# Optimization experiments

Measured on AMD Instinct MI355X. Metric: run time of the kernel, lower is better.

The kernel has to match this reference:

```python
import jax, jax.numpy as jnp
import numpy as np

B, IDF, RES = 32, 64, 128
CDF, SRC_L, A_DIM = 768, 18, 100
QUERY_L = RES * RES


def setup_inputs() -> dict:
    key = jax.random.key(0)
    ks = jax.random.split(key, 5)
    inputs = jax.random.normal(ks[0], (B, IDF, RES, RES), dtype=jnp.float32)
    context = jax.random.normal(ks[1], (B, CDF, SRC_L), dtype=jnp.float32)
    conv_ctx_w = jax.random.normal(ks[2], (IDF, CDF), dtype=jnp.float32) * (1.0 / np.sqrt(CDF))
    conv_w = jax.random.normal(ks[3], (IDF,), dtype=jnp.float32) * (1.0 / np.sqrt(IDF))
    conv_b = jnp.zeros((1,), dtype=jnp.float32)
    fc_w = jax.random.normal(ks[4], (A_DIM, QUERY_L), dtype=jnp.float32) * (1.0 / np.sqrt(QUERY_L))
    fc_b = jnp.zeros((A_DIM,), dtype=jnp.float32)
    return {"inputs": inputs, "context": context, "conv_ctx_w": conv_ctx_w,
            "conv_w": conv_w, "conv_b": conv_b, "fc_w": fc_w, "fc_b": fc_b}


def reference(inputs, context, conv_ctx_w, conv_w, conv_b, fc_w, fc_b):
    b, idf, ih, iw = inputs.shape
    queryL = ih * iw
    # target: [b, idf, queryL]
    target = inputs.reshape(b, idf, queryL)
    # 1x1 conv on context (conv_context): [b, idf, sourceL]
    sourceT = jnp.einsum('ic,bcs->bis', conv_ctx_w, context)
    # attn scores: [b, queryL, sourceL]; softmax over sourceL (dim=1 on flattened view)
    attn = jnp.einsum('biq,bis->bqs', target, sourceT)
    attn = jax.nn.softmax(attn, axis=-1)
    # weighted context: [b, idf, queryL]
    wctx = jnp.einsum('bis,bqs->biq', sourceT, attn)
    # 1x1 conv to single channel (self.conv): [b, queryL]
    wctx = jnp.einsum('i,biq->bq', conv_w, wctx) + conv_b
    # att_fc: [b, a_dim]
    out = wctx @ fc_w.T + fc_b
    return out
```

## Files before the change

kernel.cpp:

```cpp
#include <hip/hip_runtime.h>

#define BB 32
#define IDF 64
#define QL 16384
#define CDF 768
#define SL 18
#define SLP 20
#define CLP 21
#define ADIM 100

typedef __attribute__((address_space(3))) unsigned int lds_u32_t;
typedef __attribute__((address_space(1))) const unsigned int glb_u32_t;

__global__ __launch_bounds__(256, 2) void kA_source(
        const float* __restrict__ ctx,
        const float* __restrict__ wic,
        const float* __restrict__ fc_b,
        float* __restrict__ sT,
        float* __restrict__ out)
{
    __shared__ float ctx_l[CDF * CLP];
    const int blk  = blockIdx.x;
    const int tid  = threadIdx.x;
    const int wave = tid >> 6;
    const int lane = tid & 63;
    const int b = blk >> 4;
    const int g = blk & 15;

    if (blk < 13) {
        const int t = blk * 256 + tid;
        if (t < BB * ADIM) out[t] = fc_b[t % ADIM];
    }

    const float* ctxb = ctx + (size_t)b * CDF * SL;
    for (int t = tid; t < CDF * SL; t += 256) {
        const int c = t / SL;
        const int s = t - c * SL;
        ctx_l[c * CLP + s] = ctxb[t];
    }
    __syncthreads();

    const int i = g * 4 + wave;
    const float* wrow = wic + (size_t)i * CDF;

    float acc[SL];
#pragma unroll
    for (int s = 0; s < SL; s++) acc[s] = 0.f;

#pragma unroll 2
    for (int k = 0; k < CDF / 64; k++) {
        const int c = k * 64 + lane;
        const float wv = wrow[c];
#pragma unroll
        for (int s = 0; s < SL; s++) acc[s] += wv * ctx_l[c * CLP + s];
    }
#pragma unroll
    for (int s = 0; s < SL; s++) {
        float a = acc[s];
#pragma unroll
        for (int off = 32; off; off >>= 1) a += __shfl_xor(a, off, 64);
        if (lane == 0) sT[((size_t)b * IDF + i) * SLP + s] = a;
    }
}

__global__ __launch_bounds__(256, 4) void kB_attn(
        const float* __restrict__ inp,
        const float* __restrict__ sT,
        const float* __restrict__ conv_w,
        const float* __restrict__ conv_b,
        float* __restrict__ wq)
{
    __shared__ __align__(16) float xbuf[2][8][512];
    __shared__ float v_l[SL];
    const int b   = blockIdx.y;
    const int qt  = blockIdx.x;
    const int tid = threadIdx.x;
    const int wave = tid >> 6;
    const int lane = tid & 63;
    const float* st = sT + (size_t)b * IDF * SLP;

    if (tid < SL) {
        float a = 0.f;
        for (int i = 0; i < IDF; i++) a += conv_w[i] * st[i * SLP + tid];
        v_l[tid] = a;
    }

    const float* gbase = inp + (size_t)b * IDF * QL + (size_t)qt * 512;

#define STAGE(st_idx, buf)                                                              \
    {                                                                                   \
        const int i0_ = (st_idx) * 8;                                                   \
        _Pragma("unroll")                                                               \
        for (int c_ = 0; c_ < 4; c_++) {                                                \
            const int j_ = wave * 4 + c_;                                               \
            const int r_ = j_ >> 1, h_ = j_ & 1;                                        \
            const float* g_ = gbase + (size_t)(i0_ + r_) * QL + h_ * 256 + lane * 4;    \
            float* l_ = &xbuf[(buf)][r_][h_ * 256];                                     \
            __builtin_amdgcn_global_load_lds((glb_u32_t*)g_, (lds_u32_t*)l_, 16, 0, 0); \
        }                                                                               \
    }

    STAGE(0, 0);

    float2 sc[SL];
#pragma unroll
    for (int s = 0; s < SL; s++) sc[s] = make_float2(0.f, 0.f);

#pragma unroll 1
    for (int k = 0; k < 8; k++) {
        __syncthreads();
        if (k < 7) STAGE(k + 1, (k + 1) & 1);
        const int kb = k & 1;
#pragma unroll
        for (int r = 0; r < 8; r++) {
            const int i = k * 8 + r;
            const float x0 = xbuf[kb][r][tid];
            const float x1 = xbuf[kb][r][tid + 256];
            const float* strow = st + i * SLP;
#pragma unroll
            for (int s = 0; s < SL; s++) {
                const float rs = strow[s];
                sc[s].x += x0 * rs;
                sc[s].y += x1 * rs;
            }
        }
    }

    float2 m = sc[0];
#pragma unroll
    for (int s = 1; s < SL; s++) {
        m.x = fmaxf(m.x, sc[s].x);
        m.y = fmaxf(m.y, sc[s].y);
    }
    float2 l = make_float2(0.f, 0.f);
    float2 o = make_float2(0.f, 0.f);
#pragma unroll
    for (int s = 0; s < SL; s++) {
        const float vs = v_l[s];
        float2 p;
        p.x = __expf(sc[s].x - m.x);
        p.y = __expf(sc[s].y - m.y);
        l.x += p.x; l.y += p.y;
        o.x += p.x * vs; o.y += p.y * vs;
    }
    const float cb = conv_b[0];
    float* wqb = wq + (size_t)b * QL + (size_t)qt * 512;
    wqb[tid]       = o.x / l.x + cb;
    wqb[tid + 256] = o.y / l.y + cb;
}

__global__ __launch_bounds__(320, 2) void kC_fc(
        const float* __restrict__ wq,
        const float* __restrict__ fcw,
        float* __restrict__ out)
{
    const int blk = blockIdx.x;
    const int bg  = blk / 80;
    const int rem = blk - bg * 80;
    const int ag  = rem >> 3;
    const int qc  = rem & 7;
    const int wave = threadIdx.x >> 6;
    const int lane = threadIdx.x & 63;
    const int a0 = ag * 10 + wave * 2;
    const int b0 = bg * 8;
    const int q0 = qc * 2048;

    float acc[2][8];
#pragma unroll
    for (int j = 0; j < 2; j++)
#pragma unroll
        for (int i = 0; i < 8; i++) acc[j][i] = 0.f;

#pragma unroll 2
    for (int k = 0; k < 8; k++) {
        const int qi = q0 + (k * 64 + lane) * 4;
        float4 fv[2];
#pragma unroll
        for (int j = 0; j < 2; j++) fv[j] = *(const float4*)(fcw + (size_t)(a0 + j) * QL + qi);
        float4 wv[8];
#pragma unroll
        for (int i = 0; i < 8; i++) wv[i] = *(const float4*)(wq + (size_t)(b0 + i) * QL + qi);
#pragma unroll
        for (int j = 0; j < 2; j++)
#pragma unroll
            for (int i = 0; i < 8; i++)
                acc[j][i] += fv[j].x * wv[i].x + fv[j].y * wv[i].y
                           + fv[j].z * wv[i].z + fv[j].w * wv[i].w;
    }

#pragma unroll
    for (int j = 0; j < 2; j++) {
#pragma unroll
        for (int i = 0; i < 8; i++) {
            float r = acc[j][i];
#pragma unroll
            for (int off = 32; off; off >>= 1) r += __shfl_xor(r, off, 64);
            if (lane == 0) atomicAdd(&out[(b0 + i) * ADIM + a0 + j], r);
        }
    }
}

extern "C" void kernel_launch(void* const* d_in, const int* in_sizes, int n_in,
                              void* d_out, int out_size, void* d_ws, size_t ws_size,
                              hipStream_t stream)
{
    const float* inputs     = (const float*)d_in[0];
    const float* context    = (const float*)d_in[1];
    const float* conv_ctx_w = (const float*)d_in[2];
    const float* conv_w     = (const float*)d_in[3];
    const float* conv_b     = (const float*)d_in[4];
    const float* fc_w       = (const float*)d_in[5];
    const float* fc_b       = (const float*)d_in[6];
    float* out = (float*)d_out;

    float* ws = (float*)d_ws;
    float* sT = ws;
    float* wq = ws + (size_t)BB * IDF * SLP;

    kA_source<<<dim3(512), dim3(256), 0, stream>>>(context, conv_ctx_w, fc_b, sT, out);
    kB_attn<<<dim3(32, BB), dim3(256), 0, stream>>>(inputs, sT, conv_w, conv_b, wq);
    kC_fc<<<dim3(320), dim3(320), 0, stream>>>(wq, fc_w, out);
}
```

Before: 233.7 us.

## Fuse FC projection into attention kernel, drop intermediate wq buffer

Each attention block keeps its 512 softmax-weighted outputs in LDS and immediately computes the partial dot products with the matching fc_w slice for all 100 outputs, accumulating via atomics. This removes the third kernel launch and the global write/read of the wq intermediate. In exchange fc_w is re-read once per batch (from L2), and the number of atomic adds grows substantially.

```diff
diff --git a/kernel.cpp b/kernel.cpp
--- a/kernel.cpp
+++ b/kernel.cpp
@@ -68,10 +68,12 @@
         const float* __restrict__ sT,
         const float* __restrict__ conv_w,
         const float* __restrict__ conv_b,
-        float* __restrict__ wq)
+        const float* __restrict__ fcw,
+        float* __restrict__ out)
 {
     __shared__ __align__(16) float xbuf[2][8][512];
     __shared__ float v_l[SL];
+    __shared__ __align__(16) float wq_l[512];
     const int b   = blockIdx.y;
     const int qt  = blockIdx.x;
     const int tid = threadIdx.x;
@@ -144,59 +146,23 @@
         o.x += p.x * vs; o.y += p.y * vs;
     }
     const float cb = conv_b[0];
-    float* wqb = wq + (size_t)b * QL + (size_t)qt * 512;
-    wqb[tid]       = o.x / l.x + cb;
-    wqb[tid + 256] = o.y / l.y + cb;
-}
+    wq_l[tid]       = o.x / l.x + cb;
+    wq_l[tid + 256] = o.y / l.y + cb;
+    __syncthreads();
 
-__global__ __launch_bounds__(320, 2) void kC_fc(
-        const float* __restrict__ wq,
-        const float* __restrict__ fcw,
-        float* __restrict__ out)
-{
-    const int blk = blockIdx.x;
-    const int bg  = blk / 80;
-    const int rem = blk - bg * 80;
-    const int ag  = rem >> 3;
-    const int qc  = rem & 7;
-    const int wave = threadIdx.x >> 6;
-    const int lane = threadIdx.x & 63;
-    const int a0 = ag * 10 + wave * 2;
-    const int b0 = bg * 8;
-    const int q0 = qc * 2048;
-
-    float acc[2][8];
+    const float4 w0 = *(const float4*)(&wq_l[lane * 4]);
+    const float4 w1 = *(const float4*)(&wq_l[256 + lane * 4]);
+    const float* fbase = fcw + (size_t)qt * 512 + lane * 4;
+#pragma unroll 2
+    for (int j = 0; j < 25; j++) {
+        const int a = j * 4 + wave;
+        const float4 f0 = *(const float4*)(fbase + (size_t)a * QL);
+        const float4 f1 = *(const float4*)(fbase + (size_t)a * QL + 256);
+        float r = f0.x * w0.x + f0.y * w0.y + f0.z * w0.z + f0.w * w0.w
+                + f1.x * w1.x + f1.y * w1.y + f1.z * w1.z + f1.w * w1.w;
 #pragma unroll
-    for (int j = 0; j < 2; j++)
-#pragma unroll
-        for (int i = 0; i < 8; i++) acc[j][i] = 0.f;
-
-#pragma unroll 2
-    for (int k = 0; k < 8; k++) {
-        const int qi = q0 + (k * 64 + lane) * 4;
-        float4 fv[2];
-#pragma unroll
-        for (int j = 0; j < 2; j++) fv[j] = *(const float4*)(fcw + (size_t)(a0 + j) * QL + qi);
-        float4 wv[8];
-#pragma unroll
-        for (int i = 0; i < 8; i++) wv[i] = *(const float4*)(wq + (size_t)(b0 + i) * QL + qi);
-#pragma unroll
-        for (int j = 0; j < 2; j++)
-#pragma unroll
-            for (int i = 0; i < 8; i++)
-                acc[j][i] += fv[j].x * wv[i].x + fv[j].y * wv[i].y
-                           + fv[j].z * wv[i].z + fv[j].w * wv[i].w;
-    }
-
-#pragma unroll
-    for (int j = 0; j < 2; j++) {
-#pragma unroll
-        for (int i = 0; i < 8; i++) {
-            float r = acc[j][i];
-#pragma unroll
-            for (int off = 32; off; off >>= 1) r += __shfl_xor(r, off, 64);
-            if (lane == 0) atomicAdd(&out[(b0 + i) * ADIM + a0 + j], r);
-        }
+        for (int off = 32; off; off >>= 1) r += __shfl_xor(r, off, 64);
+        if (lane == 0) atomicAdd(&out[b * ADIM + a], r);
     }
 }
 
@@ -215,9 +181,7 @@
 
     float* ws = (float*)d_ws;
     float* sT = ws;
-    float* wq = ws + (size_t)BB * IDF * SLP;
 
     kA_source<<<dim3(512), dim3(256), 0, stream>>>(context, conv_ctx_w, fc_b, sT, out);
-    kB_attn<<<dim3(32, BB), dim3(256), 0, stream>>>(inputs, sT, conv_w, conv_b, wq);
-    kC_fc<<<dim3(320), dim3(320), 0, stream>>>(wq, fc_w, out);
+    kB_attn<<<dim3(32, BB), dim3(256), 0, stream>>>(inputs, sT, conv_w, conv_b, fc_w, out);
 }
```

Result: slower. 239.7 us (+2.6%).
